# Kernel tuning notes

Hardware: AMD Instinct MI355X
Metric: run time of the kernel (lower is better)

The kernel has to match this reference:

```python
import jax, jax.numpy as jnp
import numpy as np

B, C, H, W = 2, 256, 56, 56
NH = 8
HD = C // NH
SCALE = HD ** -0.5
BN_EPS = 1e-5


def _linear(x, w, b=None):
    y = jnp.einsum('...i,oi->...o', x, w)
    return y + b if b is not None else y


def _dwconv3(v, w, b):
    # depthwise 3x3, stride 1, pad 1
    y = jax.lax.conv_general_dilated(v, w, (1, 1), 'SAME',
                                     dimension_numbers=('NCHW', 'OIHW', 'NCHW'),
                                     feature_group_count=C)
    return y + b[None, :, None, None]


def _spectral(x, context, qw, kvw, pw, pb, dww, dwb):
    # SpectralCrossAttention, sr_ratio=1 path
    xt = jnp.transpose(x, (0, 2, 3, 1))                    # B,H,W,C
    q = jnp.transpose(_linear(xt, qw), (0, 3, 1, 2))       # B,C,H,W
    ct = jnp.transpose(context, (0, 2, 3, 1))
    kv = _linear(ct, kvw)                                  # B,H,W,2C -> split [2,C]
    k = jnp.transpose(kv[..., :C], (0, 3, 1, 2))
    v = jnp.transpose(kv[..., C:], (0, 3, 1, 2))
    v_local = _dwconv3(v, dww, dwb)
    qf = jnp.fft.rfft2(q, s=(H, W), axes=(-2, -1), norm='ortho')
    kf = jnp.fft.rfft2(k, s=(H, W), axes=(-2, -1), norm='ortho')
    attn_map = jnp.fft.irfft2(qf * kf, s=(H, W), axes=(-2, -1), norm='ortho')
    out = attn_map * v + v_local
    out = _linear(jnp.transpose(out, (0, 2, 3, 1)), pw, pb)
    return jnp.transpose(out, (0, 3, 1, 2))


def _token(x, context, qw, kvw, pw, pb, cw):
    # TokenSpectralResidualCrossAttention, sr_ratio=1 path (de_conv = Identity)
    N = H * W
    xt = jnp.transpose(x.reshape(B, C, N), (0, 2, 1))       # B,N,C
    ct = jnp.transpose(context.reshape(B, C, N), (0, 2, 1))
    q = jnp.transpose(_linear(xt, qw).reshape(B, N, NH, HD), (0, 2, 1, 3))  # B,NH,N,HD
    kv = _linear(ct, kvw).reshape(B, N, 2, NH, HD)
    k = jnp.transpose(kv[:, :, 0], (0, 2, 1, 3))
    v = jnp.transpose(kv[:, :, 1], (0, 2, 1, 3))            # B,NH,N,HD
    attn = jax.nn.softmax(jnp.einsum('bhnd,bhmd->bhnm', q, k) * SCALE, axis=-1)
    x_attn = jnp.transpose(jnp.einsum('bhnm,bhmd->bhnd', attn, v), (0, 2, 1, 3)).reshape(B, N, C)
    v_img = jnp.transpose(v, (0, 1, 3, 2)).reshape(B, C, H, W)
    vf = jnp.fft.rfft2(v_img, s=(H, W), axes=(-2, -1), norm='ortho')
    weight = cw[..., 0] + 1j * cw[..., 1]                   # C,H,W//2+1 complex
    v_res = jnp.fft.irfft2(vf * weight[None], s=(H, W), axes=(-2, -1), norm='ortho')
    v_res = jnp.transpose(v_res.reshape(B, C, N), (0, 2, 1))
    out = _linear(x_attn + v_res, pw, pb)
    return jnp.transpose(out, (0, 2, 1)).reshape(B, C, H, W)


def _fuse(os_, ot, g_w1, g_bn_g, g_bn_b, g_w2, g_b2):
    # spatial_gate: Conv1x1(2C->C, no bias) -> BN(eval: mean0/var1) -> ReLU -> Conv1x1(C->1) -> Sigmoid
    g_in = jnp.concatenate([os_, ot], axis=1)               # B,2C,H,W
    h = jnp.einsum('oc,bchw->bohw', g_w1, g_in)
    h = h / jnp.sqrt(1.0 + BN_EPS) * g_bn_g[None, :, None, None] + g_bn_b[None, :, None, None]
    h = jax.nn.relu(h)
    gate = jax.nn.sigmoid(jnp.einsum('oc,bchw->bohw', g_w2, h) + g_b2[None, :, None, None])
    return gate * os_ + (1.0 - gate) * ot


def setup_inputs():
    key = jax.random.key(0)
    ks = jax.random.split(key, 14)
    p = lambda i, shape, s=0.02: jax.random.normal(ks[i], shape, jnp.float32) * s
    return {
        'x': jax.random.normal(ks[0], (B, C, H, W), jnp.float32),
        'context': jax.random.normal(ks[1], (B, C, H, W), jnp.float32),
        's_q_w': p(2, (C, C)),
        's_kv_w': p(3, (2 * C, C)),
        's_proj_w': p(4, (C, C)),
        's_proj_b': jnp.zeros((C,), jnp.float32),
        's_dw_w': p(5, (C, 1, 3, 3), float(np.sqrt(2.0 / 9.0))),
        's_dw_b': jnp.zeros((C,), jnp.float32),
        't_q_w': p(6, (C, C)),
        't_kv_w': p(7, (2 * C, C)),
        't_proj_w': p(8, (C, C)),
        't_proj_b': jnp.zeros((C,), jnp.float32),
        't_cw': p(9, (C, H, W // 2 + 1, 2)),
        'g_w1': p(10, (C, 2 * C), float(np.sqrt(2.0 / C))),
        'g_bn_g': jnp.ones((C,), jnp.float32),
        'g_bn_b': jnp.zeros((C,), jnp.float32),
        'g_w2': p(11, (1, C), float(np.sqrt(2.0 / C))),
        'g_b2': jnp.zeros((1,), jnp.float32),
    }


def reference(x, context, s_q_w, s_kv_w, s_proj_w, s_proj_b, s_dw_w, s_dw_b,
              t_q_w, t_kv_w, t_proj_w, t_proj_b, t_cw,
              g_w1, g_bn_g, g_bn_b, g_w2, g_b2):
    os_ = _spectral(x, context, s_q_w, s_kv_w, s_proj_w, s_proj_b, s_dw_w, s_dw_b)
    ot = _token(x, context, t_q_w, t_kv_w, t_proj_w, t_proj_b, t_cw)
    return _fuse(os_, ot, g_w1, g_bn_g, g_bn_b, g_w2, g_b2)
```

## Files before the change

kernel.cpp:

```cpp
#include <hip/hip_runtime.h>

namespace {
constexpr int kB = 2;
constexpr int kC = 256;
constexpr int kH = 56;
constexpr int kW = 56;
constexpr int kN = kH * kW;
constexpr int kNH = 8;
constexpr int kHD = 32;
constexpr int kNF = kW / 2 + 1;
constexpr int kSpec = kH * kNF;
constexpr long kCN = (long)kC * kN;
constexpr float kAttScale = 0.17677669529663687f;
constexpr float kLog2e = 1.4426950408889634f;
constexpr float kAng = 6.283185307179586f / 56.0f;
constexpr int TW1F = 0;
constexpr int TW2F = 8192;
constexpr int TW1I = 12288;
constexpr int TW2I = 20480;
constexpr int TWTOT = 24576;
}

typedef __attribute__((ext_vector_type(8))) short short8;
typedef __attribute__((ext_vector_type(4))) float float4v;

union Frag {
    short8 s;
    unsigned short u[8];
    uint2 u2[2];
    uint4 u4;
};

__device__ __forceinline__ unsigned short f2b(float f) {
    unsigned u = __float_as_uint(f);
    return (unsigned short)((u + 0x7FFFu + ((u >> 16) & 1u)) >> 16);
}
__device__ __forceinline__ unsigned f2b_pk(float a, float b) {
    unsigned ua = __float_as_uint(a); ua = (ua + 0x7FFFu + ((ua >> 16) & 1u)) >> 16;
    unsigned ub = __float_as_uint(b); ub = (ub + 0x7FFFu + ((ub >> 16) & 1u)) >> 16;
    return ua | (ub << 16);
}
__device__ __forceinline__ unsigned pk_trunc(float a, float b) {
    return (__float_as_uint(a) >> 16) | (__float_as_uint(b) & 0xFFFF0000u);
}
__device__ __forceinline__ uint4 pk8(const float* v) {
    return make_uint4(f2b_pk(v[0], v[1]), f2b_pk(v[2], v[3]),
                      f2b_pk(v[4], v[5]), f2b_pk(v[6], v[7]));
}

__global__ __launch_bounds__(256)
void twiddle_init_kernel(unsigned short* __restrict__ tw)
{
    int idx = blockIdx.x * 256 + threadIdx.x;
    if (idx >= TWTOT) return;
    float val = 0.f;
    if (idx < TW2F) {
        int r = idx >> 6, c = idx & 63;
        if (c < 56) {
            if (r < 56)       val = cosf(kAng * (float)((r * c) % 56));
            else if (r < 112) val = sinf(kAng * (float)(((r - 56) * c) % 56));
        }
    } else if (idx < TW1I) {
        int t = idx - TW2F; int r = t >> 6, c = t & 63;
        if (c < 56) {
            if (r < 29)                  val = cosf(kAng * (float)((r * c) % 56));
            else if (r >= 32 && r < 61)  val = sinf(kAng * (float)(((r - 32) * c) % 56));
        }
    } else if (idx < TW2I) {
        int t = idx - TW1I; int r = t >> 6, c = t & 63;
        if (c < 56) {
            if (r < 56)                  val = cosf(kAng * (float)((r * c) % 56));
            else if (r >= 64 && r < 120) val = sinf(kAng * (float)(((r - 64) * c) % 56));
        }
    } else {
        int t = idx - TW2I; int x = t >> 6, c = t & 63;
        if (x < 56 && c < 58) {
            int v = c >> 1;
            float wv = ((v == 0) || (v == 28)) ? 1.f : 2.f;
            float a = kAng * (float)((v * x) % 56);
            val = (c & 1) ? (-wv * sinf(a)) : (wv * cosf(a));
        }
    }
    tw[idx] = f2b(val);
}

__global__ __launch_bounds__(256)
void dft_fwd_mfma3(const float* __restrict__ s0, const float* __restrict__ s1,
                   const float* __restrict__ s2, float* __restrict__ d0,
                   float* __restrict__ d1, float* __restrict__ d2,
                   const unsigned short* __restrict__ tw)
{
    const int bx = blockIdx.x;
    const int which = bx >> 9, ch = bx & 511;
    const int b = ch >> 8, c = ch & 255;
    const float* src; long stride; float* spec;
    if (which == 0)      { src = s0; stride = kCN;     spec = d0; }
    else if (which == 1) { src = s1; stride = 2 * kCN; spec = d1; }
    else                 { src = s2; stride = 2 * kCN; spec = d2; }
    const float* img = src + (long)b * stride + (long)c * kN;

    __shared__ __align__(16) char smem[48128];
    unsigned short (*Gb)[72]   = (unsigned short(*)[72])smem;
    unsigned short (*imgT)[72] = (unsigned short(*)[72])(smem + 18432);
    float (*Yb)[116]           = (float(*)[116])(smem + 18432);

    const int tid = threadIdx.x;
    const int wave = tid >> 6, lane = tid & 63;
    const int ln = lane & 15, qd = lane >> 4;

    for (int i = tid; i < 64 * 72; i += 256) {
        int r = i / 72, cc = i - r * 72;
        if (r >= 56 || cc >= 56) imgT[r][cc] = 0;
    }
    for (int i = tid; i < kN; i += 256) {
        int y = i / 56, x = i - y * 56;
        imgT[x][y] = f2b(img[i]);
    }
    __syncthreads();

    float4v acc1[2][4];
#pragma unroll
    for (int m = 0; m < 2; ++m)
#pragma unroll
        for (int n = 0; n < 4; ++n) acc1[m][n] = (float4v){0.f, 0.f, 0.f, 0.f};
#pragma unroll
    for (int ks = 0; ks < 2; ++ks) {
        Frag a[2], bf[4];
#pragma unroll
        for (int m = 0; m < 2; ++m)
            a[m].u4 = *(const uint4*)(tw + TW1F + ((2 * wave + m) * 16 + ln) * 64 + ks * 32 + qd * 8);
#pragma unroll
        for (int n = 0; n < 4; ++n)
            bf[n].u4 = *(const uint4*)&imgT[n * 16 + ln][ks * 32 + qd * 8];
#pragma unroll
        for (int m = 0; m < 2; ++m)
#pragma unroll
            for (int n = 0; n < 4; ++n)
                acc1[m][n] = __builtin_amdgcn_mfma_f32_16x16x32_bf16(a[m].s, bf[n].s, acc1[m][n], 0, 0, 0);
    }
#pragma unroll
    for (int m = 0; m < 2; ++m)
#pragma unroll
        for (int n = 0; n < 4; ++n)
#pragma unroll
            for (int r = 0; r < 4; ++r)
                Gb[(2 * wave + m) * 16 + qd * 4 + r][n * 16 + ln] = f2b(acc1[m][n][r]);
    __syncthreads();

    float4v acc2[7];
#pragma unroll
    for (int n = 0; n < 7; ++n) acc2[n] = (float4v){0.f, 0.f, 0.f, 0.f};
#pragma unroll
    for (int ks = 0; ks < 2; ++ks) {
        Frag a;
        a.u4 = *(const uint4*)(tw + TW2F + (wave * 16 + ln) * 64 + ks * 32 + qd * 8);
#pragma unroll
        for (int n = 0; n < 7; ++n) {
            Frag bb;
            bb.u4 = *(const uint4*)&Gb[n * 16 + ln][ks * 32 + qd * 8];
            acc2[n] = __builtin_amdgcn_mfma_f32_16x16x32_bf16(a.s, bb.s, acc2[n], 0, 0, 0);
        }
    }
#pragma unroll
    for (int n = 0; n < 7; ++n)
#pragma unroll
        for (int r = 0; r < 4; ++r)
            Yb[wave * 16 + qd * 4 + r][n * 16 + ln] = acc2[n][r];
    __syncthreads();

    float2* outp = (float2*)spec + (long)ch * kSpec;
    for (int i = tid; i < kSpec; i += 256) {
        int u = i / kNF, v = i - u * kNF;
        float Qr = Yb[v][u] - Yb[32 + v][56 + u];
        float Qi = -Yb[32 + v][u] - Yb[v][56 + u];
        outp[i] = make_float2(Qr, Qi);
    }
}

__global__ __launch_bounds__(256)
void dft_inv_mfma2(const float* __restrict__ fQ, const float* __restrict__ fK,
                   const float* __restrict__ fV, const float* __restrict__ cw,
                   float* __restrict__ dst1, float* __restrict__ dst2,
                   const float* __restrict__ skvp, const float* __restrict__ dww,
                   const float* __restrict__ dwb, const unsigned short* __restrict__ tw)
{
    const int unit = blockIdx.x >> 9;
    const int ch = blockIdx.x & 511;
    const int b = ch >> 8, c = ch & 255;
    __shared__ __align__(16) char smem[41984];
    unsigned short (*Pb)[72] = (unsigned short(*)[72])smem;
    float (*Yb)[64]          = (float(*)[64])(smem + 9216);
    unsigned short (*T2)[72] = (unsigned short(*)[72])smem;
    float (*svs)[65]         = (float(*)[65])(smem + 9216);

    const int tid = threadIdx.x;
    const int wave = tid >> 6, lane = tid & 63;
    const int ln = lane & 15, qd = lane >> 4;

    const float2* Pin; const float2* Min; float scale; float* dst;
    if (unit == 0) {
        Pin = (const float2*)fQ + (long)ch * kSpec;
        Min = (const float2*)fK + (long)ch * kSpec;
        scale = 1.0f / 175616.0f; dst = dst1;
    } else {
        Pin = (const float2*)fV + (long)ch * kSpec;
        Min = (const float2*)cw + (long)c * kSpec;
        scale = 1.0f / 3136.0f; dst = dst2;
    }

    for (int i = tid; i < 64 * 72; i += 256) {
        int r = i / 72, cc = i - r * 72;
        if (r >= 58 || cc >= 56) Pb[r][cc] = 0;
    }
    for (int i = tid; i < kSpec; i += 256) {
        int u = i / kNF, v = i - u * kNF;
        float2 p = Pin[i];
        float2 m = Min[i];
        float pr = (p.x * m.x - p.y * m.y) * scale;
        float pi = (p.x * m.y + p.y * m.x) * scale;
        Pb[2 * v][u]     = f2b(pr);
        Pb[2 * v + 1][u] = f2b(pi);
    }
    __syncthreads();

    float4v acc1[2][4];
#pragma unroll
    for (int m = 0; m < 2; ++m)
#pragma unroll
        for (int n = 0; n < 4; ++n) acc1[m][n] = (float4v){0.f, 0.f, 0.f, 0.f};
#pragma unroll
    for (int ks = 0; ks < 2; ++ks) {
        Frag a[2], bf[4];
#pragma unroll
        for (int m = 0; m < 2; ++m)
            a[m].u4 = *(const uint4*)(tw + TW1I + ((2 * wave + m) * 16 + ln) * 64 + ks * 32 + qd * 8);
#pragma unroll
        for (int n = 0; n < 4; ++n)
            bf[n].u4 = *(const uint4*)&Pb[n * 16 + ln][ks * 32 + qd * 8];
#pragma unroll
        for (int m = 0; m < 2; ++m)
#pragma unroll
            for (int n = 0; n < 4; ++n)
                acc1[m][n] = __builtin_amdgcn_mfma_f32_16x16x32_bf16(a[m].s, bf[n].s, acc1[m][n], 0, 0, 0);
    }
#pragma unroll
    for (int m = 0; m < 2; ++m)
#pragma unroll
        for (int n = 0; n < 4; ++n)
#pragma unroll
            for (int r = 0; r < 4; ++r)
                Yb[(2 * wave + m) * 16 + qd * 4 + r][n * 16 + ln] = acc1[m][n][r];
    __syncthreads();

    for (int i = tid; i < 64 * 72; i += 256) {
        int r = i / 72, cc = i - r * 72;
        if (r >= 56 || cc >= 58) T2[r][cc] = 0;
    }
    __syncthreads();
    for (int i = tid; i < 56 * kNF; i += 256) {
        int y = i / kNF, v = i - y * kNF;
        float Tr = Yb[y][2 * v]     - Yb[64 + y][2 * v + 1];
        float Ti = Yb[y][2 * v + 1] + Yb[64 + y][2 * v];
        T2[y][2 * v]     = f2b(Tr);
        T2[y][2 * v + 1] = f2b(Ti);
    }
    __syncthreads();

    float wreg[9]; float bias = 0.f;
    if (unit == 0) {
        const float* svp = skvp + (long)b * 2 * kCN + kCN + (long)c * kN;
        for (int i = tid; i < 58 * 65; i += 256) {
            int y = i / 65, x = i - y * 65;
            if (y == 0 || y == 57 || x == 0 || x >= 57) ((float*)svs)[i] = 0.f;
        }
        for (int i = tid; i < kN; i += 256) {
            int y = i / 56, x = i - y * 56;
            svs[y + 1][x + 1] = svp[i];
        }
#pragma unroll
        for (int j = 0; j < 9; ++j) wreg[j] = dww[c * 9 + j];
        bias = dwb[c];
    }

    float4v acc2[4];
#pragma unroll
    for (int n = 0; n < 4; ++n) acc2[n] = (float4v){0.f, 0.f, 0.f, 0.f};
#pragma unroll
    for (int ks = 0; ks < 2; ++ks) {
        Frag a;
        a.u4 = *(const uint4*)(tw + TW2I + (wave * 16 + ln) * 64 + ks * 32 + qd * 8);
#pragma unroll
        for (int n = 0; n < 4; ++n) {
            Frag bb;
            bb.u4 = *(const uint4*)&T2[n * 16 + ln][ks * 32 + qd * 8];
            acc2[n] = __builtin_amdgcn_mfma_f32_16x16x32_bf16(a.s, bb.s, acc2[n], 0, 0, 0);
        }
    }
    __syncthreads();

    float* outd = dst + (long)ch * kN;
#pragma unroll
    for (int n = 0; n < 4; ++n) {
        int y = n * 16 + ln;
        if (y < 56) {
#pragma unroll
            for (int r = 0; r < 4; ++r) {
                int x = wave * 16 + qd * 4 + r;
                if (x < 56) {
                    int e = y * 56 + x;
                    if (unit == 0) {
                        float s = bias;
                        s = fmaf(wreg[0], svs[y][x],     s);
                        s = fmaf(wreg[1], svs[y][x + 1], s);
                        s = fmaf(wreg[2], svs[y][x + 2], s);
                        s = fmaf(wreg[3], svs[y + 1][x],     s);
                        s = fmaf(wreg[4], svs[y + 1][x + 1], s);
                        s = fmaf(wreg[5], svs[y + 1][x + 2], s);
                        s = fmaf(wreg[6], svs[y + 2][x],     s);
                        s = fmaf(wreg[7], svs[y + 2][x + 1], s);
                        s = fmaf(wreg[8], svs[y + 2][x + 2], s);
                        outd[e] = fmaf(acc2[n][r], svs[y + 1][x + 1], s);
                    } else {
                        outd[e] = acc2[n][r];
                    }
                }
            }
        }
    }
}

__global__ __launch_bounds__(256)
void gemm_fused(const float* __restrict__ W0, const float* __restrict__ W1,
                const float* __restrict__ X0, const float* __restrict__ X1,
                const float* __restrict__ b0, const float* __restrict__ b1,
                float* __restrict__ Y0, float* __restrict__ Y1,
                int oHalf, int CI, long xbs, long ybs, int oOffset)
{
    const int b  = blockIdx.z;
    const int sel = blockIdx.y >= oHalf;
    const int o0 = (sel ? blockIdx.y - oHalf : blockIdx.y) * 64;
    const int oY = o0 + (sel ? oOffset : 0);
    const int n0 = blockIdx.x * 128;
    const float* Wm = sel ? W1 : W0;
    const float* bias = sel ? b1 : b0;
    const float* Xb = (sel ? X1 : X0) + (long)b * xbs;
    float* Yb = (sel ? Y1 : Y0) + (long)b * ybs;

    __shared__ __align__(16) unsigned short Wt[64][40];
    __shared__ __align__(16) unsigned short Xt[128][40];

    const int tid = threadIdx.x;
    const int wave = tid >> 6, lane = tid & 63;
    const int ln = lane & 15, qd = lane >> 4;
    const int wy = wave >> 1, wx = wave & 1;

    const int ow = tid >> 2, kcw = tid & 3;
    const int nx = tid & 127, kcx = tid >> 7;
    const bool xvalid = (n0 + nx) < kN;

    float4v acc[2][4];
#pragma unroll
    for (int i = 0; i < 2; ++i)
#pragma unroll
        for (int j = 0; j < 4; ++j) acc[i][j] = (float4v){0.f, 0.f, 0.f, 0.f};

    float wpre[8], xpre[16];
    {
        const float* ws = Wm + (long)(o0 + ow) * CI + kcw * 8;
        *(float4*)&wpre[0] = *(const float4*)ws;
        *(float4*)&wpre[4] = *(const float4*)(ws + 4);
#pragma unroll
        for (int j = 0; j < 16; ++j)
            xpre[j] = xvalid ? Xb[(long)(kcx * 16 + j) * kN + n0 + nx] : 0.f;
    }

    for (int k0 = 0; k0 < CI; k0 += 32) {
        *(uint4*)&Wt[ow][kcw * 8]      = pk8(wpre);
        *(uint4*)&Xt[nx][kcx * 16]     = pk8(xpre);
        *(uint4*)&Xt[nx][kcx * 16 + 8] = pk8(xpre + 8);
        __syncthreads();

        if (k0 + 32 < CI) {
            const float* ws = Wm + (long)(o0 + ow) * CI + k0 + 32 + kcw * 8;
            *(float4*)&wpre[0] = *(const float4*)ws;
            *(float4*)&wpre[4] = *(const float4*)(ws + 4);
#pragma unroll
            for (int j = 0; j < 16; ++j)
                xpre[j] = xvalid ? Xb[(long)(k0 + 32 + kcx * 16 + j) * kN + n0 + nx] : 0.f;
        }

        Frag af[2], bf4[4];
#pragma unroll
        for (int mt = 0; mt < 2; ++mt)
            af[mt].u4 = *(const uint4*)&Wt[wy * 32 + mt * 16 + ln][qd * 8];
#pragma unroll
        for (int nt = 0; nt < 4; ++nt)
            bf4[nt].u4 = *(const uint4*)&Xt[wx * 64 + nt * 16 + ln][qd * 8];
#pragma unroll
        for (int mt = 0; mt < 2; ++mt)
#pragma unroll
            for (int nt = 0; nt < 4; ++nt)
                acc[mt][nt] = __builtin_amdgcn_mfma_f32_16x16x32_bf16(
                    af[mt].s, bf4[nt].s, acc[mt][nt], 0, 0, 0);
        __syncthreads();
    }

#pragma unroll
    for (int mt = 0; mt < 2; ++mt) {
        const int obL = o0 + wy * 32 + mt * 16 + qd * 4;
        const int obY = oY + wy * 32 + mt * 16 + qd * 4;
#pragma unroll
        for (int nt = 0; nt < 4; ++nt) {
            const int n = n0 + wx * 64 + nt * 16 + ln;
            if (n < kN) {
#pragma unroll
                for (int r = 0; r < 4; ++r) {
                    float v = acc[mt][nt][r];
                    if (bias) v += bias[obL + r];
                    Yb[(long)(obY + r) * kN + n] = v;
                }
            }
        }
    }
}

__global__ __launch_bounds__(256)
void gemm_bn_kernel(const float* __restrict__ Wm, const float* __restrict__ X,
                    const float* __restrict__ gamma, const float* __restrict__ beta,
                    float* __restrict__ Y, int CI, long xbs, long ybs)
{
    const int b  = blockIdx.z;
    const int o0 = blockIdx.y * 64;
    const int n0 = blockIdx.x * 128;
    const float* Xb = X + (long)b * xbs;
    float* Yb = Y + (long)b * ybs;

    __shared__ __align__(16) unsigned short Wt[64][40];
    __shared__ __align__(16) unsigned short Xt[128][40];

    const int tid = threadIdx.x;
    const int wave = tid >> 6, lane = tid & 63;
    const int ln = lane & 15, qd = lane >> 4;
    const int wy = wave >> 1, wx = wave & 1;

    const int ow = tid >> 2, kcw = tid & 3;
    const int nx = tid & 127, kcx = tid >> 7;
    const bool xvalid = (n0 + nx) < kN;

    float4v acc[2][4];
#pragma unroll
    for (int i = 0; i < 2; ++i)
#pragma unroll
        for (int j = 0; j < 4; ++j) acc[i][j] = (float4v){0.f, 0.f, 0.f, 0.f};

    float wpre[8], xpre[16];
    {
        const float* ws = Wm + (long)(o0 + ow) * CI + kcw * 8;
        *(float4*)&wpre[0] = *(const float4*)ws;
        *(float4*)&wpre[4] = *(const float4*)(ws + 4);
#pragma unroll
        for (int j = 0; j < 16; ++j)
            xpre[j] = xvalid ? Xb[(long)(kcx * 16 + j) * kN + n0 + nx] : 0.f;
    }

    for (int k0 = 0; k0 < CI; k0 += 32) {
        *(uint4*)&Wt[ow][kcw * 8]      = pk8(wpre);
        *(uint4*)&Xt[nx][kcx * 16]     = pk8(xpre);
        *(uint4*)&Xt[nx][kcx * 16 + 8] = pk8(xpre + 8);
        __syncthreads();

        if (k0 + 32 < CI) {
            const float* ws = Wm + (long)(o0 + ow) * CI + k0 + 32 + kcw * 8;
            *(float4*)&wpre[0] = *(const float4*)ws;
            *(float4*)&wpre[4] = *(const float4*)(ws + 4);
#pragma unroll
            for (int j = 0; j < 16; ++j)
                xpre[j] = xvalid ? Xb[(long)(k0 + 32 + kcx * 16 + j) * kN + n0 + nx] : 0.f;
        }

        Frag af[2], bf4[4];
#pragma unroll
        for (int mt = 0; mt < 2; ++mt)
            af[mt].u4 = *(const uint4*)&Wt[wy * 32 + mt * 16 + ln][qd * 8];
#pragma unroll
        for (int nt = 0; nt < 4; ++nt)
            bf4[nt].u4 = *(const uint4*)&Xt[wx * 64 + nt * 16 + ln][qd * 8];
#pragma unroll
        for (int mt = 0; mt < 2; ++mt)
#pragma unroll
            for (int nt = 0; nt < 4; ++nt)
                acc[mt][nt] = __builtin_amdgcn_mfma_f32_16x16x32_bf16(
                    af[mt].s, bf4[nt].s, acc[mt][nt], 0, 0, 0);
        __syncthreads();
    }

    const float rs = rsqrtf(1.0f + 1e-5f);
#pragma unroll
    for (int mt = 0; mt < 2; ++mt) {
        const int ob = o0 + wy * 32 + mt * 16 + qd * 4;
#pragma unroll
        for (int nt = 0; nt < 4; ++nt) {
            const int n = n0 + wx * 64 + nt * 16 + ln;
            if (n < kN) {
#pragma unroll
                for (int r = 0; r < 4; ++r) {
                    const int o = ob + r;
                    float v = fmaxf(fmaf(acc[mt][nt][r], gamma[o] * rs, beta[o]), 0.f);
                    Yb[(long)o * kN + n] = v;
                }
            }
        }
    }
}

__global__ __launch_bounds__(256)
void attn_prepack_kernel(const float* __restrict__ tkv,
                         unsigned short* __restrict__ Kp,
                         unsigned short* __restrict__ Vp)
{
    const int blk = blockIdx.x;
    const int i = blk % 49;
    const int h = (blk / 49) & 7;
    const int b = blk / (49 * 8);
    const float* kb = tkv + (long)b * 2 * kCN + (long)h * kHD * kN;
    const float* vb = kb + kCN;
    const int tid = threadIdx.x;

    __shared__ float Ks[32][72];
#pragma unroll
    for (int j = 0; j < 8; ++j) {
        int e = tid + j * 256;
        int d = e >> 6, c = e & 63;
        Ks[d][c] = kb[(long)d * kN + i * 64 + c];
    }
    __syncthreads();
    {
        int tl = tid >> 6, lnn = (tid >> 2) & 15, qdd = tid & 3;
        float v[8];
#pragma unroll
        for (int j = 0; j < 8; ++j) v[j] = Ks[qdd * 8 + j][tl * 16 + lnn];
        unsigned short* dst = Kp + ((long)(b * 8 + h) * 196 + 4 * i + tl) * 512 + lnn * 32 + qdd * 8;
        *(uint4*)dst = pk8(v);
    }
    {
        int g = tid >> 7, dh = (tid >> 6) & 1, lnn = (tid >> 2) & 15, qdd = tid & 3;
        int d = dh * 16 + lnn;
        const float* src = vb + (long)d * kN + i * 64 + g * 32 + qdd * 8;
        float v[8];
        *(float4*)&v[0] = *(const float4*)src;
        *(float4*)&v[4] = *(const float4*)(src + 4);
        unsigned short* dst = Vp + ((long)(b * 8 + h) * 49 + i) * 2048 + ((g * 2 + dh) * 16 + lnn) * 32 + qdd * 8;
        *(uint4*)dst = pk8(v);
    }
}

__global__ __launch_bounds__(256)
void attn_mfma_kernel(const float* __restrict__ tq,
                      const unsigned short* __restrict__ Kp,
                      const unsigned short* __restrict__ Vp,
                      float* __restrict__ Op, float* __restrict__ lp)
{
    const int b = blockIdx.z >> 2, sp = blockIdx.z & 3;
    const int h = blockIdx.y;
    const int q0 = blockIdx.x * 128;
    const int tid = threadIdx.x;
    const int wave = tid >> 6, lane = tid & 63;
    const int qd = lane >> 4, ln = lane & 15;
    const int i0 = (sp == 0) ? 0 : (12 * sp + 1);
    const int i1 = 12 * sp + 13;

    const float* qb = tq + (long)b * kCN + (long)h * kHD * kN;
    const unsigned short* KpB = Kp + (long)(b * 8 + h) * 196 * 512 + ln * 32 + qd * 8;
    const unsigned short* VpB = Vp + (long)(b * 8 + h) * 49 * 2048 + ln * 32 + qd * 8;

    __shared__ __align__(16) unsigned short Ps[4][32 * 40];
    unsigned short* PsW = Ps[wave];

    const float qscale = kAttScale * kLog2e;
    Frag qf[2];
#pragma unroll
    for (int qt = 0; qt < 2; ++qt) {
        int qg = q0 + wave * 32 + qt * 16 + ln;
        bool qv = qg < kN;
#pragma unroll
        for (int j = 0; j < 8; ++j) {
            int d = qd * 8 + j;
            float v = qv ? qb[(long)d * kN + qg] * qscale : 0.f;
            qf[qt].u[j] = f2b(v);
        }
    }

    float4v o[2][2];
#pragma unroll
    for (int qt = 0; qt < 2; ++qt)
#pragma unroll
        for (int dh = 0; dh < 2; ++dh) o[qt][dh] = (float4v){0.f, 0.f, 0.f, 0.f};
    float lsum[2] = {0.f, 0.f};

    Frag ka[4];
#pragma unroll
    for (int m = 0; m < 4; ++m)
        ka[m].u4 = *(const uint4*)(KpB + (long)(4 * i0 + m) * 512);

    for (int i = i0; i < i1; ++i) {
        Frag va[2][2];
#pragma unroll
        for (int g = 0; g < 2; ++g)
#pragma unroll
            for (int dh = 0; dh < 2; ++dh)
                va[g][dh].u4 = *(const uint4*)(VpB + (long)i * 2048 + (g * 2 + dh) * 512);

        float4v st[4][2];
#pragma unroll
        for (int m = 0; m < 4; ++m)
#pragma unroll
            for (int qt = 0; qt < 2; ++qt)
                st[m][qt] = __builtin_amdgcn_mfma_f32_16x16x32_bf16(
                    ka[m].s, qf[qt].s, (float4v){0.f, 0.f, 0.f, 0.f}, 0, 0, 0);

        if (i + 1 < i1) {
#pragma unroll
            for (int m = 0; m < 4; ++m)
                ka[m].u4 = *(const uint4*)(KpB + (long)(4 * (i + 1) + m) * 512);
        }

#pragma unroll
        for (int m = 0; m < 4; ++m)
#pragma unroll
            for (int qt = 0; qt < 2; ++qt) {
                float e0 = __builtin_amdgcn_exp2f(st[m][qt][0]);
                float e1 = __builtin_amdgcn_exp2f(st[m][qt][1]);
                float e2 = __builtin_amdgcn_exp2f(st[m][qt][2]);
                float e3 = __builtin_amdgcn_exp2f(st[m][qt][3]);
                lsum[qt] += (e0 + e1) + (e2 + e3);
                uint2 w = make_uint2(pk_trunc(e0, e1), pk_trunc(e2, e3));
                *(uint2*)&PsW[(qt * 16 + ln) * 40 + m * 16 + qd * 4] = w;
            }

#pragma unroll
        for (int g = 0; g < 2; ++g) {
            Frag pa[2];
#pragma unroll
            for (int qt = 0; qt < 2; ++qt)
                pa[qt].u4 = *(const uint4*)&PsW[(qt * 16 + ln) * 40 + g * 32 + qd * 8];
#pragma unroll
            for (int qt = 0; qt < 2; ++qt)
#pragma unroll
                for (int dh = 0; dh < 2; ++dh)
                    o[qt][dh] = __builtin_amdgcn_mfma_f32_16x16x32_bf16(
                        pa[qt].s, va[g][dh].s, o[qt][dh], 0, 0, 0);
        }
    }

    const long grp = (long)(sp * 16 + b * 8 + h);
#pragma unroll
    for (int qt = 0; qt < 2; ++qt) {
        lsum[qt] += __shfl_xor(lsum[qt], 16, 64);
        lsum[qt] += __shfl_xor(lsum[qt], 32, 64);
        if (qd == 0)
            lp[grp * 3200 + q0 + wave * 32 + qt * 16 + ln] = lsum[qt];
#pragma unroll
        for (int dh = 0; dh < 2; ++dh)
#pragma unroll
            for (int r = 0; r < 4; ++r) {
                int q = q0 + wave * 32 + qt * 16 + qd * 4 + r;
                Op[(grp * 3200 + q) * 32 + dh * 16 + ln] = o[qt][dh][r];
            }
    }
}

__global__ __launch_bounds__(256)
void attn_combine_kernel(const float* __restrict__ Op, const float* __restrict__ lp,
                         float* __restrict__ xo)
{
    const int qc = blockIdx.x, bh = blockIdx.y;
    const int b = bh >> 3, h = bh & 7;
    const int q0 = qc * 64;
    __shared__ float T[32][65];
    const int tid = threadIdx.x;

    for (int i = tid; i < 64 * 32; i += 256) {
        int ql = i >> 5, d = i & 31;
        float ov = 0.f, l = 0.f;
#pragma unroll
        for (int s = 0; s < 4; ++s) {
            long g = (long)(s * 16 + bh);
            ov += Op[(g * 3200 + q0 + ql) * 32 + d];
            l  += lp[g * 3200 + q0 + ql];
        }
        T[d][ql] = ov / l;
    }
    __syncthreads();
    for (int i = tid; i < 32 * 64; i += 256) {
        int d = i >> 6, ql = i & 63;
        xo[(long)b * kCN + (long)(h * kHD + d) * kN + q0 + ql] += T[d][ql];
    }
}

__global__ __launch_bounds__(256)
void gate_kernel(const float* __restrict__ hbuf, const float* __restrict__ w2,
                 const float* __restrict__ b2, float* __restrict__ gate)
{
    const int n0 = blockIdx.x * 64;
    const int b = blockIdx.y;
    const int lane = threadIdx.x & 63;
    const int g = threadIdx.x >> 6;
    const float* hb = hbuf + (long)b * kCN + n0 + lane;
    float s = 0.f;
#pragma unroll 8
    for (int c = g * 64; c < g * 64 + 64; ++c)
        s = fmaf(w2[c], hb[(long)c * kN], s);
    __shared__ float red[4][64];
    red[g][lane] = s;
    __syncthreads();
    if (g == 0) {
        float t = red[0][lane] + red[1][lane] + red[2][lane] + red[3][lane];
        gate[(long)b * kN + n0 + lane] = 1.f / (1.f + __expf(-(t + b2[0])));
    }
}

__global__ __launch_bounds__(256)
void blend_kernel(const float* __restrict__ gcat, const float* __restrict__ gate,
                  float* __restrict__ out)
{
    long e = (long)blockIdx.x * 256 + threadIdx.x;
    if (e >= (long)kB * kCN) return;
    long b = e / kCN, r = e - b * kCN;
    long n = r % kN;
    float g = gate[b * kN + n];
    float os = gcat[b * 2 * kCN + r];
    float ot = gcat[b * 2 * kCN + kCN + r];
    out[e] = g * os + (1.f - g) * ot;
}

extern "C" void kernel_launch(void* const* d_in, const int* in_sizes, int n_in,
                              void* d_out, int out_size, void* d_ws, size_t ws_size,
                              hipStream_t stream)
{
    const float* x      = (const float*)d_in[0];
    const float* ctx    = (const float*)d_in[1];
    const float* s_q_w  = (const float*)d_in[2];
    const float* s_kv_w = (const float*)d_in[3];
    const float* s_p_w  = (const float*)d_in[4];
    const float* s_p_b  = (const float*)d_in[5];
    const float* s_dw_w = (const float*)d_in[6];
    const float* s_dw_b = (const float*)d_in[7];
    const float* t_q_w  = (const float*)d_in[8];
    const float* t_kv_w = (const float*)d_in[9];
    const float* t_p_w  = (const float*)d_in[10];
    const float* t_p_b  = (const float*)d_in[11];
    const float* t_cw   = (const float*)d_in[12];
    const float* g_w1   = (const float*)d_in[13];
    const float* g_bn_g = (const float*)d_in[14];
    const float* g_bn_b = (const float*)d_in[15];
    const float* g_w2   = (const float*)d_in[16];
    const float* g_b2   = (const float*)d_in[17];
    float* out = (float*)d_out;

    float* ws = (float*)d_ws;
    const long SPEC2 = (long)kB * kC * kSpec * 2;
    float* sq   = ws;
    float* skv  = sq   + kB * kCN;
    float* tq   = skv  + kB * 2 * kCN;
    float* tkv  = tq   + kB * kCN;
    float* vloc = tkv  + kB * 2 * kCN;
    float* fQ   = vloc + kB * kCN;
    float* fK   = fQ   + SPEC2;
    float* fV   = fK   + SPEC2;
    float* gcat = fV   + SPEC2;
    float* gate = gcat + kB * 2 * kCN;
    unsigned short* tw = (unsigned short*)(gate + kB * kN);
    unsigned short* Kp = tw + TWTOT;
    unsigned short* Vp = Kp + (long)16 * 196 * 512;
    float* Opart = (float*)(Vp + (long)16 * 49 * 2048);
    float* lpart = Opart + (long)64 * 3200 * 32;

    dim3 blk(256, 1, 1);
    const int EW = (int)((long)kB * kCN / 256);

    twiddle_init_kernel<<<dim3(TWTOT / 256), blk, 0, stream>>>(tw);

    gemm_fused<<<dim3(25, 8, kB), blk, 0, stream>>>(
        s_q_w, t_q_w, x, x, nullptr, nullptr, sq, tq, 4, kC, kCN, kCN, 0);
    gemm_fused<<<dim3(25, 16, kB), blk, 0, stream>>>(
        s_kv_w, t_kv_w, ctx, ctx, nullptr, nullptr, skv, tkv, 8, kC, kCN, 2 * kCN, 0);

    dft_fwd_mfma3<<<dim3(3 * kB * kC), blk, 0, stream>>>(sq, skv, tkv + kCN, fQ, fK, fV, tw);

    dft_inv_mfma2<<<dim3(2 * kB * kC), blk, 0, stream>>>(
        fQ, fK, fV, t_cw, vloc, sq, skv, s_dw_w, s_dw_b, tw);

    attn_prepack_kernel<<<dim3(kB * kNH * 49), blk, 0, stream>>>(tkv, Kp, Vp);
    attn_mfma_kernel<<<dim3(25, kNH, 4 * kB), blk, 0, stream>>>(tq, Kp, Vp, Opart, lpart);
    attn_combine_kernel<<<dim3(49, 16), blk, 0, stream>>>(Opart, lpart, sq);

    gemm_fused<<<dim3(25, 8, kB), blk, 0, stream>>>(
        s_p_w, t_p_w, vloc, sq, s_p_b, t_p_b, gcat, gcat, 4, kC, kCN, 2 * kCN, 256);

    gemm_bn_kernel<<<dim3(25, 4, kB), blk, 0, stream>>>(g_w1, gcat, g_bn_g, g_bn_b, tkv, 2 * kC, 2 * kCN, kCN);
    gate_kernel<<<dim3(49, kB), blk, 0, stream>>>(tkv, g_w2, g_b2, gate);
    blend_kernel<<<dim3(EW), blk, 0, stream>>>(gcat, gate, out);
}
```

Before: 285.7 us.

## Merge prepack into forward DFT, pipeline attention softmax, fuse gate with blend

New measurement: 281.5 us. About the same (-1.5%).

```diff
diff --git a/kernel.cpp b/kernel.cpp
--- a/kernel.cpp
+++ b/kernel.cpp
@@ -84,13 +84,12 @@
     tw[idx] = f2b(val);
 }
 
-__global__ __launch_bounds__(256)
-void dft_fwd_mfma3(const float* __restrict__ s0, const float* __restrict__ s1,
-                   const float* __restrict__ s2, float* __restrict__ d0,
-                   float* __restrict__ d1, float* __restrict__ d2,
-                   const unsigned short* __restrict__ tw)
-{
-    const int bx = blockIdx.x;
+__device__ void dft_fwd_body(char* smem, int bx,
+                             const float* __restrict__ s0, const float* __restrict__ s1,
+                             const float* __restrict__ s2, float* __restrict__ d0,
+                             float* __restrict__ d1, float* __restrict__ d2,
+                             const unsigned short* __restrict__ tw)
+{
     const int which = bx >> 9, ch = bx & 511;
     const int b = ch >> 8, c = ch & 255;
     const float* src; long stride; float* spec;
@@ -99,7 +98,6 @@
     else                 { src = s2; stride = 2 * kCN; spec = d2; }
     const float* img = src + (long)b * stride + (long)c * kN;
 
-    __shared__ __align__(16) char smem[48128];
     unsigned short (*Gb)[72]   = (unsigned short(*)[72])smem;
     unsigned short (*imgT)[72] = (unsigned short(*)[72])(smem + 18432);
     float (*Yb)[116]           = (float(*)[116])(smem + 18432);
@@ -175,6 +173,60 @@
         float Qi = -Yb[32 + v][u] - Yb[v][56 + u];
         outp[i] = make_float2(Qr, Qi);
     }
+}
+
+__device__ void prepack_body(char* smem, int blk, const float* __restrict__ tkv,
+                             unsigned short* __restrict__ Kp,
+                             unsigned short* __restrict__ Vp)
+{
+    const int i = blk % 49;
+    const int h = (blk / 49) & 7;
+    const int b = blk / (49 * 8);
+    const float* kb = tkv + (long)b * 2 * kCN + (long)h * kHD * kN;
+    const float* vb = kb + kCN;
+    const int tid = threadIdx.x;
+
+    float (*Ks)[72] = (float(*)[72])smem;
+#pragma unroll
+    for (int j = 0; j < 8; ++j) {
+        int e = tid + j * 256;
+        int d = e >> 6, c = e & 63;
+        Ks[d][c] = kb[(long)d * kN + i * 64 + c];
+    }
+    __syncthreads();
+    {
+        int tl = tid >> 6, lnn = (tid >> 2) & 15, qdd = tid & 3;
+        float v[8];
+#pragma unroll
+        for (int j = 0; j < 8; ++j) v[j] = Ks[qdd * 8 + j][tl * 16 + lnn];
+        unsigned short* dst = Kp + ((long)(b * 8 + h) * 196 + 4 * i + tl) * 512 + lnn * 32 + qdd * 8;
+        *(uint4*)dst = pk8(v);
+    }
+    {
+        int g = tid >> 7, dh = (tid >> 6) & 1, lnn = (tid >> 2) & 15, qdd = tid & 3;
+        int d = dh * 16 + lnn;
+        const float* src = vb + (long)d * kN + i * 64 + g * 32 + qdd * 8;
+        float v[8];
+        *(float4*)&v[0] = *(const float4*)src;
+        *(float4*)&v[4] = *(const float4*)(src + 4);
+        unsigned short* dst = Vp + ((long)(b * 8 + h) * 49 + i) * 2048 + ((g * 2 + dh) * 16 + lnn) * 32 + qdd * 8;
+        *(uint4*)dst = pk8(v);
+    }
+}
+
+__global__ __launch_bounds__(256)
+void fwd3_prepack_kernel(const float* __restrict__ s0, const float* __restrict__ s1,
+                         const float* __restrict__ s2, float* __restrict__ d0,
+                         float* __restrict__ d1, float* __restrict__ d2,
+                         const unsigned short* __restrict__ tw,
+                         const float* __restrict__ tkv,
+                         unsigned short* __restrict__ Kp, unsigned short* __restrict__ Vp)
+{
+    __shared__ __align__(16) char smem[48128];
+    if (blockIdx.x < 1536)
+        dft_fwd_body(smem, blockIdx.x, s0, s1, s2, d0, d1, d2, tw);
+    else
+        prepack_body(smem, blockIdx.x - 1536, tkv, Kp, Vp);
 }
 
 __global__ __launch_bounds__(256)
@@ -513,48 +565,7 @@
     }
 }
 
-__global__ __launch_bounds__(256)
-void attn_prepack_kernel(const float* __restrict__ tkv,
-                         unsigned short* __restrict__ Kp,
-                         unsigned short* __restrict__ Vp)
-{
-    const int blk = blockIdx.x;
-    const int i = blk % 49;
-    const int h = (blk / 49) & 7;
-    const int b = blk / (49 * 8);
-    const float* kb = tkv + (long)b * 2 * kCN + (long)h * kHD * kN;
-    const float* vb = kb + kCN;
-    const int tid = threadIdx.x;
-
-    __shared__ float Ks[32][72];
-#pragma unroll
-    for (int j = 0; j < 8; ++j) {
-        int e = tid + j * 256;
-        int d = e >> 6, c = e & 63;
-        Ks[d][c] = kb[(long)d * kN + i * 64 + c];
-    }
-    __syncthreads();
-    {
-        int tl = tid >> 6, lnn = (tid >> 2) & 15, qdd = tid & 3;
-        float v[8];
-#pragma unroll
-        for (int j = 0; j < 8; ++j) v[j] = Ks[qdd * 8 + j][tl * 16 + lnn];
-        unsigned short* dst = Kp + ((long)(b * 8 + h) * 196 + 4 * i + tl) * 512 + lnn * 32 + qdd * 8;
-        *(uint4*)dst = pk8(v);
-    }
-    {
-        int g = tid >> 7, dh = (tid >> 6) & 1, lnn = (tid >> 2) & 15, qdd = tid & 3;
-        int d = dh * 16 + lnn;
-        const float* src = vb + (long)d * kN + i * 64 + g * 32 + qdd * 8;
-        float v[8];
-        *(float4*)&v[0] = *(const float4*)src;
-        *(float4*)&v[4] = *(const float4*)(src + 4);
-        unsigned short* dst = Vp + ((long)(b * 8 + h) * 49 + i) * 2048 + ((g * 2 + dh) * 16 + lnn) * 32 + qdd * 8;
-        *(uint4*)dst = pk8(v);
-    }
-}
-
-__global__ __launch_bounds__(256)
+__global__ __launch_bounds__(256, 4)
 void attn_mfma_kernel(const float* __restrict__ tq,
                       const unsigned short* __restrict__ Kp,
                       const unsigned short* __restrict__ Vp,
@@ -597,11 +608,43 @@
         for (int dh = 0; dh < 2; ++dh) o[qt][dh] = (float4v){0.f, 0.f, 0.f, 0.f};
     float lsum[2] = {0.f, 0.f};
 
+    unsigned W[4][2][2];
     Frag ka[4];
 #pragma unroll
     for (int m = 0; m < 4; ++m)
         ka[m].u4 = *(const uint4*)(KpB + (long)(4 * i0 + m) * 512);
 
+    auto computeW = [&]() {
+#pragma unroll
+        for (int m = 0; m < 4; ++m) {
+            float4v s0 = __builtin_amdgcn_mfma_f32_16x16x32_bf16(
+                ka[m].s, qf[0].s, (float4v){0.f, 0.f, 0.f, 0.f}, 0, 0, 0);
+            float4v s1 = __builtin_amdgcn_mfma_f32_16x16x32_bf16(
+                ka[m].s, qf[1].s, (float4v){0.f, 0.f, 0.f, 0.f}, 0, 0, 0);
+            float a0 = __builtin_amdgcn_exp2f(s0[0]);
+            float a1 = __builtin_amdgcn_exp2f(s0[1]);
+            float a2 = __builtin_amdgcn_exp2f(s0[2]);
+            float a3 = __builtin_amdgcn_exp2f(s0[3]);
+            lsum[0] += (a0 + a1) + (a2 + a3);
+            W[m][0][0] = pk_trunc(a0, a1);
+            W[m][0][1] = pk_trunc(a2, a3);
+            float b0 = __builtin_amdgcn_exp2f(s1[0]);
+            float b1 = __builtin_amdgcn_exp2f(s1[1]);
+            float b2 = __builtin_amdgcn_exp2f(s1[2]);
+            float b3 = __builtin_amdgcn_exp2f(s1[3]);
+            lsum[1] += (b0 + b1) + (b2 + b3);
+            W[m][1][0] = pk_trunc(b0, b1);
+            W[m][1][1] = pk_trunc(b2, b3);
+        }
+    };
+
+    computeW();
+    if (i0 + 1 < i1) {
+#pragma unroll
+        for (int m = 0; m < 4; ++m)
+            ka[m].u4 = *(const uint4*)(KpB + (long)(4 * (i0 + 1) + m) * 512);
+    }
+
     for (int i = i0; i < i1; ++i) {
         Frag va[2][2];
 #pragma unroll
@@ -610,32 +653,21 @@
             for (int dh = 0; dh < 2; ++dh)
                 va[g][dh].u4 = *(const uint4*)(VpB + (long)i * 2048 + (g * 2 + dh) * 512);
 
-        float4v st[4][2];
 #pragma unroll
         for (int m = 0; m < 4; ++m)
 #pragma unroll
             for (int qt = 0; qt < 2; ++qt)
-                st[m][qt] = __builtin_amdgcn_mfma_f32_16x16x32_bf16(
-                    ka[m].s, qf[qt].s, (float4v){0.f, 0.f, 0.f, 0.f}, 0, 0, 0);
+                *(uint2*)&PsW[(qt * 16 + ln) * 40 + m * 16 + qd * 4] =
+                    make_uint2(W[m][qt][0], W[m][qt][1]);
 
         if (i + 1 < i1) {
-#pragma unroll
-            for (int m = 0; m < 4; ++m)
-                ka[m].u4 = *(const uint4*)(KpB + (long)(4 * (i + 1) + m) * 512);
-        }
-
-#pragma unroll
-        for (int m = 0; m < 4; ++m)
-#pragma unroll
-            for (int qt = 0; qt < 2; ++qt) {
-                float e0 = __builtin_amdgcn_exp2f(st[m][qt][0]);
-                float e1 = __builtin_amdgcn_exp2f(st[m][qt][1]);
-                float e2 = __builtin_amdgcn_exp2f(st[m][qt][2]);
-                float e3 = __builtin_amdgcn_exp2f(st[m][qt][3]);
-                lsum[qt] += (e0 + e1) + (e2 + e3);
-                uint2 w = make_uint2(pk_trunc(e0, e1), pk_trunc(e2, e3));
-                *(uint2*)&PsW[(qt * 16 + ln) * 40 + m * 16 + qd * 4] = w;
+            computeW();
+            if (i + 2 < i1) {
+#pragma unroll
+                for (int m = 0; m < 4; ++m)
+                    ka[m].u4 = *(const uint4*)(KpB + (long)(4 * (i + 2) + m) * 512);
             }
+        }
 
 #pragma unroll
         for (int g = 0; g < 2; ++g) {
@@ -698,8 +730,9 @@
 }
 
 __global__ __launch_bounds__(256)
-void gate_kernel(const float* __restrict__ hbuf, const float* __restrict__ w2,
-                 const float* __restrict__ b2, float* __restrict__ gate)
+void gateblend_kernel(const float* __restrict__ hbuf, const float* __restrict__ w2,
+                      const float* __restrict__ b2, const float* __restrict__ gcat,
+                      float* __restrict__ out)
 {
     const int n0 = blockIdx.x * 64;
     const int b = blockIdx.y;
@@ -711,26 +744,23 @@
     for (int c = g * 64; c < g * 64 + 64; ++c)
         s = fmaf(w2[c], hb[(long)c * kN], s);
     __shared__ float red[4][64];
+    __shared__ float sgate[64];
     red[g][lane] = s;
     __syncthreads();
     if (g == 0) {
         float t = red[0][lane] + red[1][lane] + red[2][lane] + red[3][lane];
-        gate[(long)b * kN + n0 + lane] = 1.f / (1.f + __expf(-(t + b2[0])));
-    }
-}
-
-__global__ __launch_bounds__(256)
-void blend_kernel(const float* __restrict__ gcat, const float* __restrict__ gate,
-                  float* __restrict__ out)
-{
-    long e = (long)blockIdx.x * 256 + threadIdx.x;
-    if (e >= (long)kB * kCN) return;
-    long b = e / kCN, r = e - b * kCN;
-    long n = r % kN;
-    float g = gate[b * kN + n];
-    float os = gcat[b * 2 * kCN + r];
-    float ot = gcat[b * 2 * kCN + kCN + r];
-    out[e] = g * os + (1.f - g) * ot;
+        sgate[lane] = 1.f / (1.f + __expf(-(t + b2[0])));
+    }
+    __syncthreads();
+    const float gt = sgate[lane];
+    const float* osp = gcat + (long)b * 2 * kCN + n0 + lane;
+    const float* otp = osp + kCN;
+    float* op = out + (long)b * kCN + n0 + lane;
+    for (int c = g; c < kC; c += 4) {
+        float os = osp[(long)c * kN];
+        float ot = otp[(long)c * kN];
+        op[(long)c * kN] = gt * os + (1.f - gt) * ot;
+    }
 }
 
 extern "C" void kernel_launch(void* const* d_in, const int* in_sizes, int n_in,
@@ -776,7 +806,6 @@
     float* lpart = Opart + (long)64 * 3200 * 32;
 
     dim3 blk(256, 1, 1);
-    const int EW = (int)((long)kB * kCN / 256);
 
     twiddle_init_kernel<<<dim3(TWTOT / 256), blk, 0, stream>>>(tw);
 
@@ -785,12 +814,12 @@
     gemm_fused<<<dim3(25, 16, kB), blk, 0, stream>>>(
         s_kv_w, t_kv_w, ctx, ctx, nullptr, nullptr, skv, tkv, 8, kC, kCN, 2 * kCN, 0);
 
-    dft_fwd_mfma3<<<dim3(3 * kB * kC), blk, 0, stream>>>(sq, skv, tkv + kCN, fQ, fK, fV, tw);
+    fwd3_prepack_kernel<<<dim3(3 * kB * kC + kB * kNH * 49), blk, 0, stream>>>(
+        sq, skv, tkv + kCN, fQ, fK, fV, tw, tkv, Kp, Vp);
 
     dft_inv_mfma2<<<dim3(2 * kB * kC), blk, 0, stream>>>(
         fQ, fK, fV, t_cw, vloc, sq, skv, s_dw_w, s_dw_b, tw);
 
-    attn_prepack_kernel<<<dim3(kB * kNH * 49), blk, 0, stream>>>(tkv, Kp, Vp);
     attn_mfma_kernel<<<dim3(25, kNH, 4 * kB), blk, 0, stream>>>(tq, Kp, Vp, Opart, lpart);
     attn_combine_kernel<<<dim3(49, 16), blk, 0, stream>>>(Opart, lpart, sq);
 
@@ -798,6 +827,5 @@
         s_p_w, t_p_w, vloc, sq, s_p_b, t_p_b, gcat, gcat, 4, kC, kCN, 2 * kCN, 256);
 
     gemm_bn_kernel<<<dim3(25, 4, kB), blk, 0, stream>>>(g_w1, gcat, g_bn_g, g_bn_b, tkv, 2 * kC, 2 * kCN, kCN);
-    gate_kernel<<<dim3(49, kB), blk, 0, stream>>>(tkv, g_w2, g_b2, gate);
-    blend_kernel<<<dim3(EW), blk, 0, stream>>>(gcat, gate, out);
-}
+    gateblend_kernel<<<dim3(49, kB), blk, 0, stream>>>(tkv, g_w2, g_b2, gcat, out);
+}
```
